# Kernel optimization log

Hardware: AMD Instinct MI355X
Metric: run time of the kernel (lower is better)

Reference implementation:

```python
import jax, jax.numpy as jnp
import numpy as np

TINY = np.finfo(np.float32).tiny


def setup_inputs() -> dict:
    key = jax.random.key(0)
    k1, k2, k3 = jax.random.split(key, 3)
    B, IN, OUT = 4096, 4096, 1024
    x = jax.random.normal(k1, (B, IN), dtype=jnp.float32)
    weight = jax.random.normal(k2, (IN, OUT), dtype=jnp.float32)
    uniform = jax.random.uniform(k3, (IN, OUT), dtype=jnp.float32)
    T = jnp.ones((1,), dtype=jnp.float32)
    return {"x": x, "weight": weight, "uniform": uniform, "T": T}


def reference(x, weight, uniform, T):
    # training-path forward of ConcreteLayer
    # uniform -> (1 - tiny) * u + tiny, then Gumbel noise
    u = (1.0 - TINY) * uniform + TINY
    gumbel = -jnp.log(-jnp.log(u))                      # [in, out]
    noisy_logits = (weight + gumbel) / T                # temperature scaling
    samples = jax.nn.softmax(noisy_logits, axis=1)      # softmax over out dim (torch default for 2D)
    out = jnp.einsum('bi,ik->bk', x, samples)           # [batch, out]
    return out
```

## Files before the change

### kernel.cpp

```cpp
#include <hip/hip_runtime.h>
#include <cstdint>
#include <cstddef>


#define TINYF 1.17549435082228750797e-38f
#define LN2F 0.69314718055994530942f
#define LOG2EF 1.44269504088896340736f

typedef unsigned short u16;
typedef __attribute__((ext_vector_type(8))) short bf16x8;
typedef __attribute__((ext_vector_type(4))) float f32x4;

__device__ __forceinline__ u16 f2bf(float f) {
  union { float f; uint32_t u; } v; v.f = f;
  uint32_t r = v.u + 0x7FFFu + ((v.u >> 16) & 1u);
  return (u16)(r >> 16);
}

__device__ __forceinline__ float log2_hw(float x) { return __builtin_amdgcn_logf(x); }
__device__ __forceinline__ float exp2_hw(float x) { return __builtin_amdgcn_exp2f(x); }

__device__ __forceinline__ float gumbel_fast(float u) {
  float t = -log2_hw(u);
  return -LN2F * log2_hw(t * LN2F);
}
__device__ __forceinline__ float exp_fast(float x) { return exp2_hw(x * LOG2EF); }

__device__ __forceinline__ void gld_lds16(const void* g, void* l) {
  __builtin_amdgcn_global_load_lds(
      (__attribute__((address_space(1))) void*)(g),
      (__attribute__((address_space(3))) void*)(l), 16, 0, 0);
}

__global__ void trans_exp_kernel(const float* __restrict__ W, const float* __restrict__ U,
                                 const float* __restrict__ Tp, u16* __restrict__ BT,
                                 float* __restrict__ d) {
  __shared__ float tile[64][65];
  const int k0 = blockIdx.x * 64, n0 = blockIdx.y * 64;
  const int t = threadIdx.x;
  const float invT = 1.0f / Tp[0];
  {
    const int nn4 = (t & 15) * 4, kq = t >> 4;
#pragma unroll
    for (int r = 0; r < 4; ++r) {
      int kk = r * 16 + kq;
      size_t gi = (size_t)(k0 + kk) * 1024 + (n0 + nn4);
      float4 w = *(const float4*)&W[gi];
      float4 u = *(const float4*)&U[gi];
      float e0 = exp_fast((w.x + gumbel_fast(u.x * (1.0f - TINYF) + TINYF)) * invT);
      float e1 = exp_fast((w.y + gumbel_fast(u.y * (1.0f - TINYF) + TINYF)) * invT);
      float e2 = exp_fast((w.z + gumbel_fast(u.z * (1.0f - TINYF) + TINYF)) * invT);
      float e3 = exp_fast((w.w + gumbel_fast(u.w * (1.0f - TINYF) + TINYF)) * invT);
      tile[kk][nn4 + 0] = e0; tile[kk][nn4 + 1] = e1;
      tile[kk][nn4 + 2] = e2; tile[kk][nn4 + 3] = e3;
      float s = (e0 + e1) + (e2 + e3);
#pragma unroll
      for (int m = 8; m > 0; m >>= 1) s += __shfl_xor(s, m, 16);
      if ((t & 15) == 0) atomicAdd(&d[k0 + kk], s);
    }
  }
  __syncthreads();
  {
    const int kk4 = (t & 15) * 4, nq = t >> 4;
#pragma unroll
    for (int r = 0; r < 4; ++r) {
      int nn = r * 16 + nq;
      ushort4 o;
      o.x = f2bf(tile[kk4 + 0][nn]);
      o.y = f2bf(tile[kk4 + 1][nn]);
      o.z = f2bf(tile[kk4 + 2][nn]);
      o.w = f2bf(tile[kk4 + 3][nn]);
      *(ushort4*)&BT[(size_t)(n0 + nn) * 4096 + (k0 + kk4)] = o;
    }
  }
}

__global__ void cast_zero_kernel(const float4* __restrict__ x, const float4* __restrict__ d4,
                                 ushort4* __restrict__ xb, float4* __restrict__ out,
                                 int n4x, int n4o) {
  int i = blockIdx.x * blockDim.x + threadIdx.x;
  if (i < n4x) {
    int col4 = i & 1023;
    float4 v = x[i];
    float4 dd = d4[col4];
    ushort4 o;
    o.x = f2bf(v.x / dd.x); o.y = f2bf(v.y / dd.y);
    o.z = f2bf(v.z / dd.z); o.w = f2bf(v.w / dd.w);
    xb[i] = o;
  } else {
    int j = i - n4x;
    if (j < n4o) out[j] = make_float4(0.f, 0.f, 0.f, 0.f);
  }
}

#define TM 128
#define TN 128
#define TK 64

__launch_bounds__(256)
__global__ void gemm_bt_kernel(const u16* __restrict__ A, const u16* __restrict__ BT,
                               float* __restrict__ C, int M, int N, int K) {
  __shared__ u16 As[TM * TK];
  __shared__ u16 Bs[TN * TK];

  const int tid = threadIdx.x;
  const int lane = tid & 63, w = tid >> 6;
  const int wm = w >> 1, wn = w & 1;
  const int m0 = blockIdx.x * TM, n0 = blockIdx.y * TN;
  const int quad = lane >> 4, r16 = lane & 15;
  const int srow = lane >> 3;
  const int sg = (lane & 7) ^ srow;

  const int kz = blockIdx.z;
  const int Kh = K >> 1;
  const u16* Ak = A + (size_t)kz * Kh;
  const u16* Bk = BT + (size_t)kz * Kh;

  f32x4 acc[4][4] = {};

  for (int kt = 0; kt < Kh; kt += TK) {
    __syncthreads();
#pragma unroll
    for (int c = 0; c < 4; ++c) {
      int chunk = w * 4 + c;
      gld_lds16(Ak + (size_t)(m0 + chunk * 8 + srow) * K + kt + sg * 8, (char*)As + chunk * 1024);
      gld_lds16(Bk + (size_t)(n0 + chunk * 8 + srow) * K + kt + sg * 8, (char*)Bs + chunk * 1024);
    }
    __syncthreads();

#pragma unroll
    for (int ss = 0; ss < 2; ++ss) {
      bf16x8 aF[4], bF[4];
#pragma unroll
      for (int mi = 0; mi < 4; ++mi) {
        int row = wm * 64 + mi * 16 + r16;
        aF[mi] = *(const bf16x8*)((const char*)As + row * 128 + (((ss * 4 + quad) ^ (row & 7)) * 16));
      }
#pragma unroll
      for (int ni = 0; ni < 4; ++ni) {
        int row = wn * 64 + ni * 16 + r16;
        bF[ni] = *(const bf16x8*)((const char*)Bs + row * 128 + (((ss * 4 + quad) ^ (row & 7)) * 16));
      }
#pragma unroll
      for (int mi = 0; mi < 4; ++mi)
#pragma unroll
        for (int ni = 0; ni < 4; ++ni)
          acc[mi][ni] = __builtin_amdgcn_mfma_f32_16x16x32_bf16(aF[mi], bF[ni], acc[mi][ni], 0, 0, 0);
    }
  }

#pragma unroll
  for (int mi = 0; mi < 4; ++mi)
#pragma unroll
    for (int ni = 0; ni < 4; ++ni)
#pragma unroll
      for (int r = 0; r < 4; ++r) {
        int row = m0 + wm * 64 + mi * 16 + quad * 4 + r;
        int col = n0 + wn * 64 + ni * 16 + r16;
        atomicAdd(&C[(size_t)row * N + col], acc[mi][ni][r]);
      }
}

extern "C" void kernel_launch(void* const* d_in, const int* in_sizes, int n_in,
                              void* d_out, int out_size, void* d_ws, size_t ws_size,
                              hipStream_t stream) {
  const int M = 4096, K = 4096, N = 1024;
  const float* x = (const float*)d_in[0];
  const float* W = (const float*)d_in[1];
  const float* U = (const float*)d_in[2];
  const float* Tp = (const float*)d_in[3];
  float* out = (float*)d_out;

  char* ws = (char*)d_ws;
  u16* xb = (u16*)ws;
  u16* bt = (u16*)(ws + (size_t)M * K * 2);
  float* dsum = (float*)(ws + (size_t)M * K * 2 + (size_t)N * K * 2);

  hipMemsetAsync(dsum, 0, K * sizeof(float), stream);
  trans_exp_kernel<<<dim3(K / 64, N / 64), 256, 0, stream>>>(W, U, Tp, bt, dsum);
  const int n4x = M * K / 4, n4o = M * N / 4;
  cast_zero_kernel<<<dim3((n4x + n4o) / 256), 256, 0, stream>>>(
      (const float4*)x, (const float4*)dsum, (ushort4*)xb, (float4*)out, n4x, n4o);
  gemm_bt_kernel<<<dim3(M / TM, N / TN, 2), 256, 0, stream>>>(xb, bt, out, M, N, K);
}
```

Before: 196.6 us.

## Fuse x scaling and bf16 cast into GEMM A-load, move output zeroing

Removes the separate cast kernel: the GEMM now reads fp32 x directly, scales each element by the reciprocal of the softmax denominator, converts to bf16 and stores it into swizzled LDS. Zeroing of the output moves into the exp/transpose kernel. Split-K grows from 2 to 4 and launch bounds request 3 blocks per CU. This avoids writing and re-reading a 32MB bf16 copy of x and one kernel launch. In exchange, each GEMM block re-reads fp32 x (twice the bytes of bf16) through registers instead of async LDS loads, and doubles the atomic adds to the output.

```diff
diff --git a/kernel.cpp b/kernel.cpp
--- a/kernel.cpp
+++ b/kernel.cpp
@@ -19,6 +19,7 @@
 
 __device__ __forceinline__ float log2_hw(float x) { return __builtin_amdgcn_logf(x); }
 __device__ __forceinline__ float exp2_hw(float x) { return __builtin_amdgcn_exp2f(x); }
+__device__ __forceinline__ float rcp_hw(float x) { return __builtin_amdgcn_rcpf(x); }
 
 __device__ __forceinline__ float gumbel_fast(float u) {
   float t = -log2_hw(u);
@@ -34,11 +35,19 @@
 
 __global__ void trans_exp_kernel(const float* __restrict__ W, const float* __restrict__ U,
                                  const float* __restrict__ Tp, u16* __restrict__ BT,
-                                 float* __restrict__ d) {
+                                 float* __restrict__ d, float4* __restrict__ out4) {
   __shared__ float tile[64][65];
   const int k0 = blockIdx.x * 64, n0 = blockIdx.y * 64;
   const int t = threadIdx.x;
   const float invT = 1.0f / Tp[0];
+
+  {
+    int bid = blockIdx.y * gridDim.x + blockIdx.x;
+    float4 z = make_float4(0.f, 0.f, 0.f, 0.f);
+#pragma unroll
+    for (int j = 0; j < 4; ++j) out4[(size_t)bid * 1024 + j * 256 + t] = z;
+  }
+
   {
     const int nn4 = (t & 15) * 4, kq = t >> 4;
 #pragma unroll
@@ -75,31 +84,15 @@
   }
 }
 
-__global__ void cast_zero_kernel(const float4* __restrict__ x, const float4* __restrict__ d4,
-                                 ushort4* __restrict__ xb, float4* __restrict__ out,
-                                 int n4x, int n4o) {
-  int i = blockIdx.x * blockDim.x + threadIdx.x;
-  if (i < n4x) {
-    int col4 = i & 1023;
-    float4 v = x[i];
-    float4 dd = d4[col4];
-    ushort4 o;
-    o.x = f2bf(v.x / dd.x); o.y = f2bf(v.y / dd.y);
-    o.z = f2bf(v.z / dd.z); o.w = f2bf(v.w / dd.w);
-    xb[i] = o;
-  } else {
-    int j = i - n4x;
-    if (j < n4o) out[j] = make_float4(0.f, 0.f, 0.f, 0.f);
-  }
-}
-
 #define TM 128
 #define TN 128
 #define TK 64
-
-__launch_bounds__(256)
-__global__ void gemm_bt_kernel(const u16* __restrict__ A, const u16* __restrict__ BT,
-                               float* __restrict__ C, int M, int N, int K) {
+#define SPLITK 4
+
+__launch_bounds__(256, 3)
+__global__ void gemm_fused_kernel(const float* __restrict__ X, const float* __restrict__ dsum,
+                                  const u16* __restrict__ BT, float* __restrict__ C,
+                                  int M, int N, int K) {
   __shared__ u16 As[TM * TK];
   __shared__ u16 Bs[TN * TK];
 
@@ -110,21 +103,49 @@
   const int quad = lane >> 4, r16 = lane & 15;
   const int srow = lane >> 3;
   const int sg = (lane & 7) ^ srow;
+  const int arow = tid >> 3;
+  const int gb = tid & 7;
+  const int aslot = (gb ^ (arow & 7)) * 16;
 
   const int kz = blockIdx.z;
-  const int Kh = K >> 1;
-  const u16* Ak = A + (size_t)kz * Kh;
-  const u16* Bk = BT + (size_t)kz * Kh;
+  const int Kq = K / SPLITK;
+  const float* Xk = X + (size_t)kz * Kq;
+  const u16* Bk = BT + (size_t)kz * Kq;
+  const float* dk = dsum + (size_t)kz * Kq;
 
   f32x4 acc[4][4] = {};
 
-  for (int kt = 0; kt < Kh; kt += TK) {
+  for (int kt = 0; kt < Kq; kt += TK) {
     __syncthreads();
+    float4 av[4][2];
+#pragma unroll
+    for (int p = 0; p < 4; ++p) {
+      const float* src = Xk + (size_t)(m0 + p * 32 + arow) * K + kt + gb * 8;
+      av[p][0] = *(const float4*)src;
+      av[p][1] = *(const float4*)(src + 4);
+    }
 #pragma unroll
     for (int c = 0; c < 4; ++c) {
       int chunk = w * 4 + c;
-      gld_lds16(Ak + (size_t)(m0 + chunk * 8 + srow) * K + kt + sg * 8, (char*)As + chunk * 1024);
       gld_lds16(Bk + (size_t)(n0 + chunk * 8 + srow) * K + kt + sg * 8, (char*)Bs + chunk * 1024);
+    }
+    float4 dv0 = *(const float4*)(dk + kt + gb * 8);
+    float4 dv1 = *(const float4*)(dk + kt + gb * 8 + 4);
+    float rd0x = rcp_hw(dv0.x), rd0y = rcp_hw(dv0.y), rd0z = rcp_hw(dv0.z), rd0w = rcp_hw(dv0.w);
+    float rd1x = rcp_hw(dv1.x), rd1y = rcp_hw(dv1.y), rd1z = rcp_hw(dv1.z), rd1w = rcp_hw(dv1.w);
+#pragma unroll
+    for (int p = 0; p < 4; ++p) {
+      int row = p * 32 + arow;
+      union { u16 u[8]; bf16x8 v; } pk;
+      pk.u[0] = f2bf(av[p][0].x * rd0x);
+      pk.u[1] = f2bf(av[p][0].y * rd0y);
+      pk.u[2] = f2bf(av[p][0].z * rd0z);
+      pk.u[3] = f2bf(av[p][0].w * rd0w);
+      pk.u[4] = f2bf(av[p][1].x * rd1x);
+      pk.u[5] = f2bf(av[p][1].y * rd1y);
+      pk.u[6] = f2bf(av[p][1].z * rd1z);
+      pk.u[7] = f2bf(av[p][1].w * rd1w);
+      *(bf16x8*)((char*)As + row * 128 + aslot) = pk.v;
     }
     __syncthreads();
 
@@ -172,14 +193,10 @@
   float* out = (float*)d_out;
 
   char* ws = (char*)d_ws;
-  u16* xb = (u16*)ws;
-  u16* bt = (u16*)(ws + (size_t)M * K * 2);
-  float* dsum = (float*)(ws + (size_t)M * K * 2 + (size_t)N * K * 2);
+  u16* bt = (u16*)ws;
+  float* dsum = (float*)(ws + (size_t)N * K * 2);
 
   hipMemsetAsync(dsum, 0, K * sizeof(float), stream);
-  trans_exp_kernel<<<dim3(K / 64, N / 64), 256, 0, stream>>>(W, U, Tp, bt, dsum);
-  const int n4x = M * K / 4, n4o = M * N / 4;
-  cast_zero_kernel<<<dim3((n4x + n4o) / 256), 256, 0, stream>>>(
-      (const float4*)x, (const float4*)dsum, (ushort4*)xb, (float4*)out, n4x, n4o);
-  gemm_bt_kernel<<<dim3(M / TM, N / TN, 2), 256, 0, stream>>>(xb, bt, out, M, N, K);
-}
+  trans_exp_kernel<<<dim3(K / 64, N / 64), 256, 0, stream>>>(W, U, Tp, bt, dsum, (float4*)out);
+  gemm_fused_kernel<<<dim3(M / TM, N / TN, SPLITK), 256, 0, stream>>>(x, dsum, bt, out, M, N, K);
+}
```

After: 214.2 us. 9.0% more time.

## Raise GEMM split-K to four and move output zeroing into the transform kernel

Applied to the files above, without the earlier changes.

The GEMM split-K factor goes from 2 to 4, giving 1024 blocks instead of 512 to fill more CUs, with a launch-bounds occupancy hint added. Zeroing the output moves from the cast kernel into the weight-transform kernel, one 4096-float slice per block, so the cast kernel only converts x. The per-element division in the cast is replaced by a hardware reciprocal multiply. In exchange, twice as many fp32 atomic adds hit the output, and the reciprocal is slightly less accurate than a true divide.

```diff
diff --git a/kernel.cpp b/kernel.cpp
--- a/kernel.cpp
+++ b/kernel.cpp
@@ -19,6 +19,7 @@
 
 __device__ __forceinline__ float log2_hw(float x) { return __builtin_amdgcn_logf(x); }
 __device__ __forceinline__ float exp2_hw(float x) { return __builtin_amdgcn_exp2f(x); }
+__device__ __forceinline__ float rcp_hw(float x) { return __builtin_amdgcn_rcpf(x); }
 
 __device__ __forceinline__ float gumbel_fast(float u) {
   float t = -log2_hw(u);
@@ -34,11 +35,19 @@
 
 __global__ void trans_exp_kernel(const float* __restrict__ W, const float* __restrict__ U,
                                  const float* __restrict__ Tp, u16* __restrict__ BT,
-                                 float* __restrict__ d) {
+                                 float* __restrict__ d, float4* __restrict__ out4) {
   __shared__ float tile[64][65];
   const int k0 = blockIdx.x * 64, n0 = blockIdx.y * 64;
   const int t = threadIdx.x;
   const float invT = 1.0f / Tp[0];
+
+  {
+    int bid = blockIdx.y * gridDim.x + blockIdx.x;
+    float4 z = make_float4(0.f, 0.f, 0.f, 0.f);
+#pragma unroll
+    for (int j = 0; j < 4; ++j) out4[(size_t)bid * 1024 + j * 256 + t] = z;
+  }
+
   {
     const int nn4 = (t & 15) * 4, kq = t >> 4;
 #pragma unroll
@@ -75,29 +84,25 @@
   }
 }
 
-__global__ void cast_zero_kernel(const float4* __restrict__ x, const float4* __restrict__ d4,
-                                 ushort4* __restrict__ xb, float4* __restrict__ out,
-                                 int n4x, int n4o) {
+__global__ void cast_kernel(const float4* __restrict__ x, const float4* __restrict__ d4,
+                            ushort4* __restrict__ xb, int n4x) {
   int i = blockIdx.x * blockDim.x + threadIdx.x;
-  if (i < n4x) {
-    int col4 = i & 1023;
-    float4 v = x[i];
-    float4 dd = d4[col4];
-    ushort4 o;
-    o.x = f2bf(v.x / dd.x); o.y = f2bf(v.y / dd.y);
-    o.z = f2bf(v.z / dd.z); o.w = f2bf(v.w / dd.w);
-    xb[i] = o;
-  } else {
-    int j = i - n4x;
-    if (j < n4o) out[j] = make_float4(0.f, 0.f, 0.f, 0.f);
-  }
+  if (i >= n4x) return;
+  int col4 = i & 1023;
+  float4 v = x[i];
+  float4 dd = d4[col4];
+  ushort4 o;
+  o.x = f2bf(v.x * rcp_hw(dd.x)); o.y = f2bf(v.y * rcp_hw(dd.y));
+  o.z = f2bf(v.z * rcp_hw(dd.z)); o.w = f2bf(v.w * rcp_hw(dd.w));
+  xb[i] = o;
 }
 
 #define TM 128
 #define TN 128
 #define TK 64
+#define SPLITK 4
 
-__launch_bounds__(256)
+__launch_bounds__(256, 4)
 __global__ void gemm_bt_kernel(const u16* __restrict__ A, const u16* __restrict__ BT,
                                float* __restrict__ C, int M, int N, int K) {
   __shared__ u16 As[TM * TK];
@@ -112,13 +117,13 @@
   const int sg = (lane & 7) ^ srow;
 
   const int kz = blockIdx.z;
-  const int Kh = K >> 1;
-  const u16* Ak = A + (size_t)kz * Kh;
-  const u16* Bk = BT + (size_t)kz * Kh;
+  const int Kq = K / SPLITK;
+  const u16* Ak = A + (size_t)kz * Kq;
+  const u16* Bk = BT + (size_t)kz * Kq;
 
   f32x4 acc[4][4] = {};
 
-  for (int kt = 0; kt < Kh; kt += TK) {
+  for (int kt = 0; kt < Kq; kt += TK) {
     __syncthreads();
 #pragma unroll
     for (int c = 0; c < 4; ++c) {
@@ -177,9 +182,8 @@
   float* dsum = (float*)(ws + (size_t)M * K * 2 + (size_t)N * K * 2);
 
   hipMemsetAsync(dsum, 0, K * sizeof(float), stream);
-  trans_exp_kernel<<<dim3(K / 64, N / 64), 256, 0, stream>>>(W, U, Tp, bt, dsum);
-  const int n4x = M * K / 4, n4o = M * N / 4;
-  cast_zero_kernel<<<dim3((n4x + n4o) / 256), 256, 0, stream>>>(
-      (const float4*)x, (const float4*)dsum, (ushort4*)xb, (float4*)out, n4x, n4o);
-  gemm_bt_kernel<<<dim3(M / TM, N / TN, 2), 256, 0, stream>>>(xb, bt, out, M, N, K);
+  trans_exp_kernel<<<dim3(K / 64, N / 64), 256, 0, stream>>>(W, U, Tp, bt, dsum, (float4*)out);
+  cast_kernel<<<dim3(M * K / 4 / 256), 256, 0, stream>>>((const float4*)x, (const float4*)dsum,
+                                                         (ushort4*)xb, M * K / 4);
+  gemm_bt_kernel<<<dim3(M / TM, N / TN, SPLITK), 256, 0, stream>>>(xb, bt, out, M, N, K);
 }
```

Result: slower. 212.4 us (+8.0%).
